# Kernel tuning notes

Hardware: AMD Instinct MI355X
Metric: run time of the kernel (lower is better)

## Reference

```python
import jax, jax.numpy as jnp
import numpy as np

N, E = 100000, 640000
IN_DIM, OUT_DIM, H, D = 128, 128, 4, 32  # head_dim = out_dim // num_heads
NUM_EDGE_TYPES = 3
NEG_SLOPE = 0.2


def setup_inputs() -> dict:
    key = jax.random.key(0)
    ks = jax.random.split(key, 10)
    x = jax.random.normal(ks[0], (N, IN_DIM), dtype=jnp.float32)
    edge_index = jax.random.randint(ks[1], (2, E), 0, N, dtype=jnp.int32)
    edge_type = jax.random.randint(ks[2], (E,), 0, NUM_EDGE_TYPES, dtype=jnp.int32)
    s = 1.0 / np.sqrt(IN_DIM)
    Wq = jax.random.uniform(ks[3], (IN_DIM, H * D), jnp.float32, -s, s)
    Wk = jax.random.uniform(ks[4], (IN_DIM, H * D), jnp.float32, -s, s)
    Wv = jax.random.uniform(ks[5], (IN_DIM, H * D), jnp.float32, -s, s)
    # xavier_uniform on (1, H, 2D): gain*sqrt(6/(fan_in+fan_out)) with fans (2D, H)
    a = np.sqrt(6.0 / (2 * D + H))
    attn_lin = jax.random.uniform(ks[6], (1, H, 2 * D), jnp.float32, -a, a)
    edge_embed_table = jax.random.normal(ks[7], (NUM_EDGE_TYPES, H * D), dtype=jnp.float32)
    so = 1.0 / np.sqrt(H * D)
    Wout = jax.random.uniform(ks[8], (H * D, OUT_DIM), jnp.float32, -so, so)
    bout = jax.random.uniform(ks[9], (OUT_DIM,), jnp.float32, -so, so)
    return {"x": x, "Wq": Wq, "Wk": Wk, "Wv": Wv, "attn_lin": attn_lin,
            "edge_embed_table": edge_embed_table, "Wout": Wout, "bout": bout,
            "edge_index": edge_index, "edge_type": edge_type}


def reference(x, Wq, Wk, Wv, attn_lin, edge_embed_table, Wout, bout, edge_index, edge_type):
    n = x.shape[0]
    src, dst = edge_index[0], edge_index[1]
    q = (x @ Wq).reshape(n, H, D)
    k = (x @ Wk).reshape(n, H, D)
    v = (x @ Wv).reshape(n, H, D)
    q_src = q[src]            # (E, H, D)
    k_dst = k[dst]            # (E, H, D)
    # (cat([q_src,k_dst]) * attn_lin).sum(-1) == q_src.a_q + k_dst.a_k
    a_q, a_k = attn_lin[0, :, :D], attn_lin[0, :, D:]      # (H, D) each
    scores = jnp.einsum('ehd,hd->eh', q_src, a_q) + jnp.einsum('ehd,hd->eh', k_dst, a_k)
    scores = jnp.where(scores >= 0, scores, NEG_SLOPE * scores)  # leaky_relu
    edge_embed = edge_embed_table[edge_type].reshape(-1, H, D)
    scores = scores + jnp.sum(q_src * edge_embed, axis=-1)       # (E, H)
    # segmented softmax over destination node (detached max, clamped at -100)
    m = jax.ops.segment_max(jax.lax.stop_gradient(scores), dst, num_segments=n)
    m = jnp.maximum(m, -100.0)
    ex = jnp.exp(scores - m[dst])
    denom = jax.ops.segment_sum(ex, dst, num_segments=n)
    alpha = ex / (denom[dst] + 1e-10)                            # (E, H)
    messages = alpha[:, :, None] * v[src]                        # (E, H, D)
    out = jax.ops.segment_sum(messages, dst, num_segments=n)     # (N, H, D)
    out = out.reshape(n, H * D)
    return out @ Wout + bout
```

## Files before the change

kernel.cpp:

```cpp
#include <hip/hip_runtime.h>
#include <hip/hip_bf16.h>

#define H_   4
#define D_   32
#define HD   128
#define IND  128
#define OUTD 128
#define NET  3
#define NEG  0.2f
#define CAP  2048

typedef short short8 __attribute__((ext_vector_type(8)));
typedef float f32x4  __attribute__((ext_vector_type(4)));

__device__ __forceinline__ unsigned short f2bf(float f) {
  union { __hip_bfloat16 b; unsigned short u; } x;
  x.b = __float2bfloat16(f);
  return x.u;
}

__device__ __forceinline__ short8 pack_bf8(float4 lo, float4 hi) {
  union { short8 s; unsigned short u[8]; } r;
  r.u[0] = f2bf(lo.x); r.u[1] = f2bf(lo.y); r.u[2] = f2bf(lo.z); r.u[3] = f2bf(lo.w);
  r.u[4] = f2bf(hi.x); r.u[5] = f2bf(hi.y); r.u[6] = f2bf(hi.z); r.u[7] = f2bf(hi.w);
  return r.s;
}

__global__ void k0b_pack(const float* __restrict__ Wq, const float* __restrict__ Wk,
                         const float* __restrict__ attn, const float* __restrict__ ee,
                         const float* __restrict__ Wv, const float* __restrict__ Wout,
                         unsigned short* __restrict__ Wallt,
                         unsigned short* __restrict__ Woutt,
                         int* __restrict__ gbuck, int nbuck) {
  int b = blockIdx.x, i = threadIdx.x;
  if (b == 288) {
    for (int k = i; k < nbuck; k += 128) gbuck[k] = 0;
    return;
  }
  if (b < 160) {
    int c = b;
    float val = 0.f;
    if (c < 128) {
      val = Wv[i*HD + c];
    } else {
      int cc = c - 128;
      if (cc < 4) {
        int h = cc;
        for (int d = 0; d < D_; d++) val += Wq[i*HD + h*D_ + d] * attn[h*2*D_ + d];
      } else if (cc < 16) {
        int t2 = (cc - 4) >> 2, h = (cc - 4) & 3;
        for (int d = 0; d < D_; d++) val += Wq[i*HD + h*D_ + d] * ee[t2*HD + h*D_ + d];
      } else if (cc < 20) {
        int h = cc - 16;
        for (int d = 0; d < D_; d++) val += Wk[i*HD + h*D_ + d] * attn[h*2*D_ + D_ + d];
      }
    }
    Wallt[(c*128 + i) ^ ((c & 7) << 3)] = f2bf(val);
  } else {
    int c = b - 160;
    Woutt[(c*128 + i) ^ ((c & 7) << 3)] = f2bf(Wout[i*OUTD + c]);
  }
}

__global__ __launch_bounds__(256) void k1_gemm(const float* __restrict__ x,
    const uint4* __restrict__ Wallt,
    unsigned short* __restrict__ vb, float* __restrict__ nq,
    float* __restrict__ skb, int n) {
  __shared__ uint4 ldsB[2560];
  int t = threadIdx.x;
  #pragma unroll
  for (int i = 0; i < 10; i++) ldsB[i*256 + t] = Wallt[i*256 + t];
  int wv = t >> 6, lane = t & 63;
  int l15 = lane & 15, l16 = lane >> 4;
  int base = blockIdx.x * 64;
  int arow = base + wv*16 + l15;
  int rr = min(arow, n - 1);
  const float* xr = &x[(size_t)rr*IND + l16*8];
  short8 afr[4];
  #pragma unroll
  for (int kk = 0; kk < 4; kk++) {
    float4 lo = *(const float4*)(xr + kk*32);
    float4 hi = *(const float4*)(xr + kk*32 + 4);
    afr[kk] = pack_bf8(lo, hi);
  }
  __syncthreads();
  f32x4 acc[10];
  #pragma unroll
  for (int nt = 0; nt < 10; nt++) acc[nt] = (f32x4){0.f, 0.f, 0.f, 0.f};
  #pragma unroll
  for (int nt = 0; nt < 10; nt++) {
    int bcol = nt*16 + l15;
    #pragma unroll
    for (int kk = 0; kk < 4; kk++) {
      int bytec = kk*64 + l16*16;
      short8 b = *(const short8*)((const char*)ldsB + ((bcol*256 + bytec) ^ ((bcol & 7) << 4)));
      acc[nt] = __builtin_amdgcn_mfma_f32_16x16x32_bf16(afr[kk], b, acc[nt], 0, 0, 0);
    }
  }
  int rowbase = base + wv*16 + l16*4;
  #pragma unroll
  for (int nt = 0; nt < 10; nt++) {
    int col = nt*16 + l15;
    #pragma unroll
    for (int r = 0; r < 4; r++) {
      int row = rowbase + r;
      if (row >= n) continue;
      float val = acc[nt][r];
      if (nt < 8)       vb[(size_t)row*HD + col] = f2bf(val);
      else if (nt == 8) nq[(size_t)row*16 + (col - 128)] = val;
      else { int c = col - 144; if (c < 4) skb[(size_t)row*4 + c] = val; }
    }
  }
}

__global__ __launch_bounds__(256) void k_bucket(const int* __restrict__ ei,
    const int* __restrict__ et, int* __restrict__ gbuck,
    unsigned int* __restrict__ ebuf, int E_, int nbuck, int per) {
  __shared__ int cnt[1024];
  __shared__ int base[1024];
  int t = threadIdx.x;
  for (int i = t; i < nbuck; i += 256) cnt[i] = 0;
  __syncthreads();
  int e0 = blockIdx.x * per;
  int e1 = min(e0 + per, E_);
  for (int e = e0 + t; e < e1; e += 256)
    atomicAdd(&cnt[ei[E_ + e] >> 7], 1);
  __syncthreads();
  for (int i = t; i < nbuck; i += 256) {
    int c = cnt[i];
    base[i] = c ? atomicAdd(&gbuck[i], c) : 0;
    cnt[i] = 0;
  }
  __syncthreads();
  for (int e = e0 + t; e < e1; e += 256) {
    int d = ei[E_ + e];
    int b = d >> 7;
    int pos = base[b] + atomicAdd(&cnt[b], 1);
    ebuf[(size_t)b * CAP + pos] =
        (unsigned)ei[e] | ((unsigned)et[e] << 17) | ((unsigned)(d & 127) << 19);
  }
}

__global__ __launch_bounds__(256) void k_sort(const unsigned int* __restrict__ ebuf,
    const int* __restrict__ gbuck, int* __restrict__ offsets,
    int* __restrict__ elist, int n, int E_) {
  __shared__ int cnt[128], cur[128], sc[128], red[256];
  int b = blockIdx.x, t = threadIdx.x;
  int part = 0;
  for (int i = t; i < b; i += 256) part += gbuck[i];
  red[t] = part; __syncthreads();
  for (int off = 128; off > 0; off >>= 1) {
    if (t < off) red[t] += red[t + off];
    __syncthreads();
  }
  int bb = red[0];
  int m = gbuck[b];
  if (b == 0 && t == 0) offsets[n] = E_;
  if (t < 128) cnt[t] = 0;
  __syncthreads();
  const unsigned int* eb = ebuf + (size_t)b * CAP;
  for (int i = t; i < m; i += 256)
    atomicAdd(&cnt[(eb[i] >> 19) & 127], 1);
  __syncthreads();
  if (t < 128) sc[t] = cnt[t];
  __syncthreads();
  for (int off = 1; off < 128; off <<= 1) {
    int v = (t >= off && t < 128) ? sc[t - off] : 0;
    __syncthreads();
    if (t < 128) sc[t] += v;
    __syncthreads();
  }
  if (t < 128) {
    int excl = sc[t] - cnt[t];
    cur[t] = excl;
    int dst = b * 128 + t;
    if (dst < n) offsets[dst] = bb + excl;
  }
  __syncthreads();
  for (int i = t; i < m; i += 256) {
    unsigned int w = eb[i];
    int dl = (w >> 19) & 127;
    int p = bb + atomicAdd(&cur[dl], 1);
    elist[p] = (int)((w & 0x1FFFFu) | (((w >> 17) & 3u) << 20));
  }
}

__global__ __launch_bounds__(256) void k3_agg(
    const int* __restrict__ offsets, const int* __restrict__ elist,
    const float* __restrict__ nq, const float* __restrict__ skb,
    const unsigned short* __restrict__ vb, unsigned short* __restrict__ aggb, int n) {
  int t = threadIdx.x;
  int g = t >> 4, s = t & 15;
  int dst = blockIdx.x * 16 + g;
  __shared__ float s_esc[16][17][4];
  __shared__ int s_src[16][17];
  if (dst >= n) return;
  int off0 = offsets[dst];
  int deg = offsets[dst + 1] - off0;
  int h = s >> 2;
  unsigned short* orow = &aggb[(size_t)dst*HD + s*8];
  if (deg == 0) {
    *(uint4*)orow = make_uint4(0u, 0u, 0u, 0u);
    return;
  }
  float4 sk4 = *(const float4*)(&skb[(size_t)dst*4]);
  float dp0 = 0.f, dp1 = 0.f, dp2 = 0.f, dp3 = 0.f;
  float a0=0.f,a1=0.f,a2=0.f,a3=0.f,a4=0.f,a5=0.f,a6=0.f,a7=0.f;
  for (int bas = 0; bas < deg; bas += 16) {
    int cnt = min(16, deg - bas);
    float e0 = 0.f, e1 = 0.f, e2 = 0.f, e3 = 0.f;
    int src = 0;
    if (s < cnt) {
      int p = elist[off0 + bas + s];
      src = p & 0xFFFFF;
      int ety = p >> 20;
      float4 sq4 = *(const float4*)(&nq[(size_t)src*16]);
      float4 qe4 = *(const float4*)(&nq[(size_t)src*16 + 4 + ety*4]);
      float s0 = sq4.x + sk4.x; s0 = (s0 >= 0.f ? s0 : NEG*s0) + qe4.x; e0 = __expf(s0);
      float s1 = sq4.y + sk4.y; s1 = (s1 >= 0.f ? s1 : NEG*s1) + qe4.y; e1 = __expf(s1);
      float s2 = sq4.z + sk4.z; s2 = (s2 >= 0.f ? s2 : NEG*s2) + qe4.z; e2 = __expf(s2);
      float s3 = sq4.w + sk4.w; s3 = (s3 >= 0.f ? s3 : NEG*s3) + qe4.w; e3 = __expf(s3);
      dp0 += e0; dp1 += e1; dp2 += e2; dp3 += e3;
    }
    s_src[g][s] = src;
    *(float4*)(&s_esc[g][s][0]) = make_float4(e0, e1, e2, e3);
    __builtin_amdgcn_wave_barrier();
    int e = 0;
    for (; e + 4 <= cnt; e += 4) {
      float al0 = s_esc[g][e+0][h], al1 = s_esc[g][e+1][h];
      float al2 = s_esc[g][e+2][h], al3 = s_esc[g][e+3][h];
      int se0 = s_src[g][e+0], se1 = s_src[g][e+1];
      int se2 = s_src[g][e+2], se3 = s_src[g][e+3];
      uint4 v0 = *(const uint4*)(vb + (size_t)se0*HD + s*8);
      uint4 v1 = *(const uint4*)(vb + (size_t)se1*HD + s*8);
      uint4 v2 = *(const uint4*)(vb + (size_t)se2*HD + s*8);
      uint4 v3 = *(const uint4*)(vb + (size_t)se3*HD + s*8);
      a0 += al0 * __uint_as_float(v0.x << 16);
      a1 += al0 * __uint_as_float(v0.x & 0xFFFF0000u);
      a2 += al0 * __uint_as_float(v0.y << 16);
      a3 += al0 * __uint_as_float(v0.y & 0xFFFF0000u);
      a4 += al0 * __uint_as_float(v0.z << 16);
      a5 += al0 * __uint_as_float(v0.z & 0xFFFF0000u);
      a6 += al0 * __uint_as_float(v0.w << 16);
      a7 += al0 * __uint_as_float(v0.w & 0xFFFF0000u);
      a0 += al1 * __uint_as_float(v1.x << 16);
      a1 += al1 * __uint_as_float(v1.x & 0xFFFF0000u);
      a2 += al1 * __uint_as_float(v1.y << 16);
      a3 += al1 * __uint_as_float(v1.y & 0xFFFF0000u);
      a4 += al1 * __uint_as_float(v1.z << 16);
      a5 += al1 * __uint_as_float(v1.z & 0xFFFF0000u);
      a6 += al1 * __uint_as_float(v1.w << 16);
      a7 += al1 * __uint_as_float(v1.w & 0xFFFF0000u);
      a0 += al2 * __uint_as_float(v2.x << 16);
      a1 += al2 * __uint_as_float(v2.x & 0xFFFF0000u);
      a2 += al2 * __uint_as_float(v2.y << 16);
      a3 += al2 * __uint_as_float(v2.y & 0xFFFF0000u);
      a4 += al2 * __uint_as_float(v2.z << 16);
      a5 += al2 * __uint_as_float(v2.z & 0xFFFF0000u);
      a6 += al2 * __uint_as_float(v2.w << 16);
      a7 += al2 * __uint_as_float(v2.w & 0xFFFF0000u);
      a0 += al3 * __uint_as_float(v3.x << 16);
      a1 += al3 * __uint_as_float(v3.x & 0xFFFF0000u);
      a2 += al3 * __uint_as_float(v3.y << 16);
      a3 += al3 * __uint_as_float(v3.y & 0xFFFF0000u);
      a4 += al3 * __uint_as_float(v3.z << 16);
      a5 += al3 * __uint_as_float(v3.z & 0xFFFF0000u);
      a6 += al3 * __uint_as_float(v3.w << 16);
      a7 += al3 * __uint_as_float(v3.w & 0xFFFF0000u);
    }
    for (; e < cnt; e++) {
      float a = s_esc[g][e][h];
      int se = s_src[g][e];
      uint4 vv = *(const uint4*)(vb + (size_t)se*HD + s*8);
      a0 += a * __uint_as_float(vv.x << 16);
      a1 += a * __uint_as_float(vv.x & 0xFFFF0000u);
      a2 += a * __uint_as_float(vv.y << 16);
      a3 += a * __uint_as_float(vv.y & 0xFFFF0000u);
      a4 += a * __uint_as_float(vv.z << 16);
      a5 += a * __uint_as_float(vv.z & 0xFFFF0000u);
      a6 += a * __uint_as_float(vv.w << 16);
      a7 += a * __uint_as_float(vv.w & 0xFFFF0000u);
    }
    __builtin_amdgcn_wave_barrier();
  }
  #pragma unroll
  for (int off = 1; off < 16; off <<= 1) {
    dp0 += __shfl_xor(dp0, off);
    dp1 += __shfl_xor(dp1, off);
    dp2 += __shfl_xor(dp2, off);
    dp3 += __shfl_xor(dp3, off);
  }
  float den = (h == 0) ? dp0 : (h == 1) ? dp1 : (h == 2) ? dp2 : dp3;
  float inv = 1.f / (den + 1e-10f);
  uint4 pk;
  pk.x = (unsigned)f2bf(a0*inv) | ((unsigned)f2bf(a1*inv) << 16);
  pk.y = (unsigned)f2bf(a2*inv) | ((unsigned)f2bf(a3*inv) << 16);
  pk.z = (unsigned)f2bf(a4*inv) | ((unsigned)f2bf(a5*inv) << 16);
  pk.w = (unsigned)f2bf(a6*inv) | ((unsigned)f2bf(a7*inv) << 16);
  *(uint4*)orow = pk;
}

__global__ __launch_bounds__(256) void k4_gemm(const unsigned short* __restrict__ aggb,
    const uint4* __restrict__ Woutt, const float* __restrict__ bout,
    float* __restrict__ out, int n) {
  __shared__ uint4 ldsB[2048];
  int t = threadIdx.x;
  #pragma unroll
  for (int i = 0; i < 8; i++) ldsB[i*256 + t] = Woutt[i*256 + t];
  int wv = t >> 6, lane = t & 63;
  int l15 = lane & 15, l16 = lane >> 4;
  int base = blockIdx.x * 64;
  int arow = base + wv*16 + l15;
  int rr = min(arow, n - 1);
  const unsigned short* ar = &aggb[(size_t)rr*HD + l16*8];
  short8 afr[4];
  #pragma unroll
  for (int kk = 0; kk < 4; kk++)
    afr[kk] = *(const short8*)(ar + kk*32);
  __syncthreads();
  f32x4 acc[8];
  #pragma unroll
  for (int nt = 0; nt < 8; nt++) acc[nt] = (f32x4){0.f, 0.f, 0.f, 0.f};
  #pragma unroll
  for (int nt = 0; nt < 8; nt++) {
    int bcol = nt*16 + l15;
    #pragma unroll
    for (int kk = 0; kk < 4; kk++) {
      int bytec = kk*64 + l16*16;
      short8 b = *(const short8*)((const char*)ldsB + ((bcol*256 + bytec) ^ ((bcol & 7) << 4)));
      acc[nt] = __builtin_amdgcn_mfma_f32_16x16x32_bf16(afr[kk], b, acc[nt], 0, 0, 0);
    }
  }
  int rowbase = base + wv*16 + l16*4;
  #pragma unroll
  for (int nt = 0; nt < 8; nt++) {
    int col = nt*16 + l15;
    float bv = bout[col];
    #pragma unroll
    for (int r = 0; r < 4; r++) {
      int row = rowbase + r;
      if (row < n) out[(size_t)row*OUTD + col] = acc[nt][r] + bv;
    }
  }
}

extern "C" void kernel_launch(void* const* d_in, const int* in_sizes, int n_in,
                              void* d_out, int out_size, void* d_ws, size_t ws_size,
                              hipStream_t stream) {
  const float* x    = (const float*)d_in[0];
  const float* Wq   = (const float*)d_in[1];
  const float* Wk   = (const float*)d_in[2];
  const float* Wv   = (const float*)d_in[3];
  const float* attn = (const float*)d_in[4];
  const float* ee   = (const float*)d_in[5];
  const float* Wout = (const float*)d_in[6];
  const float* bout = (const float*)d_in[7];
  const int*   ei   = (const int*)d_in[8];
  const int*   et   = (const int*)d_in[9];
  int n  = in_sizes[0] / IND;
  int E_ = in_sizes[9];
  float* out = (float*)d_out;
  int nbuck = (n + 127) >> 7;

  char* w = (char*)d_ws;
  auto alloc = [&](size_t bytes) {
    char* p = w;
    w += (bytes + 255) & ~(size_t)255;
    return p;
  };
  unsigned short* vb    = (unsigned short*)alloc((size_t)n * HD * 2);
  unsigned short* aggb  = (unsigned short*)alloc((size_t)n * HD * 2);
  float* nq       = (float*)alloc((size_t)n * 16 * 4);
  float* skb      = (float*)alloc((size_t)n * 4 * 4);
  unsigned short* Wallt = (unsigned short*)alloc(160 * 128 * 2);
  unsigned short* Woutt = (unsigned short*)alloc(128 * 128 * 2);
  unsigned int* ebuf = (unsigned int*)alloc((size_t)nbuck * CAP * 4);
  int*   gbuck    = (int*)alloc((size_t)nbuck * 4);
  int*   offsets  = (int*)alloc(((size_t)n + 1) * 4);
  int*   elist    = (int*)alloc((size_t)E_ * 4);

  k0b_pack<<<289, 128, 0, stream>>>(Wq, Wk, attn, ee, Wv, Wout, Wallt, Woutt,
                                    gbuck, nbuck);
  k1_gemm<<<(n + 63)/64, 256, 0, stream>>>(x, (const uint4*)Wallt, vb, nq, skb, n);
  int nbb = 256;
  int per = (E_ + nbb - 1) / nbb;
  k_bucket<<<nbb, 256, 0, stream>>>(ei, et, gbuck, ebuf, E_, nbuck, per);
  k_sort<<<nbuck, 256, 0, stream>>>(ebuf, gbuck, offsets, elist, n, E_);
  k3_agg<<<(n + 15)/16, 256, 0, stream>>>(offsets, elist, nq, skb, vb, aggb, n);
  k4_gemm<<<(n + 63)/64, 256, 0, stream>>>(aggb, (const uint4*)Woutt, bout, out, n);
}
```

Baseline: 107.0 us.

## Merge edge bucketing into projection GEMM launch and store node scores as bf16

The edge-bucketing kernel now runs as extra blocks of the projection GEMM launch, so the two independent stages share one launch and can overlap on the GPU. The per-node attention-score table nq is stored in bf16 instead of fp32, which halves the bytes gathered per edge in the aggregation kernel. Source offsets are also pre-shifted into row offsets so the inner gather loop does less address arithmetic. The bf16 scores lose precision before the exponent, and the dynamic 40 KB shared allocation applies to bucketing blocks too, which may limit occupancy.

```diff
diff --git a/kernel.cpp b/kernel.cpp
--- a/kernel.cpp
+++ b/kernel.cpp
@@ -25,6 +25,9 @@
   r.u[4] = f2bf(hi.x); r.u[5] = f2bf(hi.y); r.u[6] = f2bf(hi.z); r.u[7] = f2bf(hi.w);
   return r.s;
 }
+
+#define BFLO(x) __uint_as_float((x) << 16)
+#define BFHI(x) __uint_as_float((x) & 0xFFFF0000u)
 
 __global__ void k0b_pack(const float* __restrict__ Wq, const float* __restrict__ Wk,
                          const float* __restrict__ attn, const float* __restrict__ ee,
@@ -62,12 +65,42 @@
   }
 }
 
-__global__ __launch_bounds__(256) void k1_gemm(const float* __restrict__ x,
+__global__ __launch_bounds__(256) void k1b(const float* __restrict__ x,
     const uint4* __restrict__ Wallt,
-    unsigned short* __restrict__ vb, float* __restrict__ nq,
-    float* __restrict__ skb, int n) {
-  __shared__ uint4 ldsB[2560];
+    unsigned short* __restrict__ vb, unsigned short* __restrict__ nqb,
+    float* __restrict__ skb, int n, int nblk1,
+    const int* __restrict__ ei, const int* __restrict__ et,
+    int* __restrict__ gbuck, unsigned int* __restrict__ ebuf,
+    int E_, int nbuck, int per) {
+  extern __shared__ char dlds[];
   int t = threadIdx.x;
+  if (blockIdx.x >= nblk1) {
+    int* cnt  = (int*)dlds;
+    int* base = cnt + 1024;
+    for (int i = t; i < nbuck; i += 256) cnt[i] = 0;
+    __syncthreads();
+    int bb = blockIdx.x - nblk1;
+    int e0 = bb * per;
+    int e1 = min(e0 + per, E_);
+    for (int e = e0 + t; e < e1; e += 256)
+      atomicAdd(&cnt[ei[E_ + e] >> 7], 1);
+    __syncthreads();
+    for (int i = t; i < nbuck; i += 256) {
+      int c = cnt[i];
+      base[i] = c ? atomicAdd(&gbuck[i], c) : 0;
+      cnt[i] = 0;
+    }
+    __syncthreads();
+    for (int e = e0 + t; e < e1; e += 256) {
+      int d = ei[E_ + e];
+      int b = d >> 7;
+      int pos = base[b] + atomicAdd(&cnt[b], 1);
+      ebuf[(size_t)b * CAP + pos] =
+          (unsigned)ei[e] | ((unsigned)et[e] << 17) | ((unsigned)(d & 127) << 19);
+    }
+    return;
+  }
+  uint4* ldsB = (uint4*)dlds;
   #pragma unroll
   for (int i = 0; i < 10; i++) ldsB[i*256 + t] = Wallt[i*256 + t];
   int wv = t >> 6, lane = t & 63;
@@ -107,37 +140,9 @@
       if (row >= n) continue;
       float val = acc[nt][r];
       if (nt < 8)       vb[(size_t)row*HD + col] = f2bf(val);
-      else if (nt == 8) nq[(size_t)row*16 + (col - 128)] = val;
+      else if (nt == 8) nqb[((size_t)row << 4) + (col - 128)] = f2bf(val);
       else { int c = col - 144; if (c < 4) skb[(size_t)row*4 + c] = val; }
     }
-  }
-}
-
-__global__ __launch_bounds__(256) void k_bucket(const int* __restrict__ ei,
-    const int* __restrict__ et, int* __restrict__ gbuck,
-    unsigned int* __restrict__ ebuf, int E_, int nbuck, int per) {
-  __shared__ int cnt[1024];
-  __shared__ int base[1024];
-  int t = threadIdx.x;
-  for (int i = t; i < nbuck; i += 256) cnt[i] = 0;
-  __syncthreads();
-  int e0 = blockIdx.x * per;
-  int e1 = min(e0 + per, E_);
-  for (int e = e0 + t; e < e1; e += 256)
-    atomicAdd(&cnt[ei[E_ + e] >> 7], 1);
-  __syncthreads();
-  for (int i = t; i < nbuck; i += 256) {
-    int c = cnt[i];
-    base[i] = c ? atomicAdd(&gbuck[i], c) : 0;
-    cnt[i] = 0;
-  }
-  __syncthreads();
-  for (int e = e0 + t; e < e1; e += 256) {
-    int d = ei[E_ + e];
-    int b = d >> 7;
-    int pos = base[b] + atomicAdd(&cnt[b], 1);
-    ebuf[(size_t)b * CAP + pos] =
-        (unsigned)ei[e] | ((unsigned)et[e] << 17) | ((unsigned)(d & 127) << 19);
   }
 }
 
@@ -187,7 +192,7 @@
 
 __global__ __launch_bounds__(256) void k3_agg(
     const int* __restrict__ offsets, const int* __restrict__ elist,
-    const float* __restrict__ nq, const float* __restrict__ skb,
+    const unsigned short* __restrict__ nqb, const float* __restrict__ skb,
     const unsigned short* __restrict__ vb, unsigned short* __restrict__ aggb, int n) {
   int t = threadIdx.x;
   int g = t >> 4, s = t & 15;
@@ -209,77 +214,65 @@
   for (int bas = 0; bas < deg; bas += 16) {
     int cnt = min(16, deg - bas);
     float e0 = 0.f, e1 = 0.f, e2 = 0.f, e3 = 0.f;
-    int src = 0;
+    int srcoff = 0;
     if (s < cnt) {
       int p = elist[off0 + bas + s];
-      src = p & 0xFFFFF;
+      int src = p & 0xFFFFF;
       int ety = p >> 20;
-      float4 sq4 = *(const float4*)(&nq[(size_t)src*16]);
-      float4 qe4 = *(const float4*)(&nq[(size_t)src*16 + 4 + ety*4]);
-      float s0 = sq4.x + sk4.x; s0 = (s0 >= 0.f ? s0 : NEG*s0) + qe4.x; e0 = __expf(s0);
-      float s1 = sq4.y + sk4.y; s1 = (s1 >= 0.f ? s1 : NEG*s1) + qe4.y; e1 = __expf(s1);
-      float s2 = sq4.z + sk4.z; s2 = (s2 >= 0.f ? s2 : NEG*s2) + qe4.z; e2 = __expf(s2);
-      float s3 = sq4.w + sk4.w; s3 = (s3 >= 0.f ? s3 : NEG*s3) + qe4.w; e3 = __expf(s3);
+      const unsigned short* nr = nqb + ((size_t)src << 4);
+      uint2 sqp = *(const uint2*)nr;
+      uint2 qep = *(const uint2*)(nr + 4 + ety*4);
+      float s0 = BFLO(sqp.x) + sk4.x;
+      float s1 = BFHI(sqp.x) + sk4.y;
+      float s2 = BFLO(sqp.y) + sk4.z;
+      float s3 = BFHI(sqp.y) + sk4.w;
+      s0 = (s0 >= 0.f ? s0 : NEG*s0) + BFLO(qep.x); e0 = __expf(s0);
+      s1 = (s1 >= 0.f ? s1 : NEG*s1) + BFHI(qep.x); e1 = __expf(s1);
+      s2 = (s2 >= 0.f ? s2 : NEG*s2) + BFLO(qep.y); e2 = __expf(s2);
+      s3 = (s3 >= 0.f ? s3 : NEG*s3) + BFHI(qep.y); e3 = __expf(s3);
       dp0 += e0; dp1 += e1; dp2 += e2; dp3 += e3;
-    }
-    s_src[g][s] = src;
+      srcoff = src << 7;
+    }
+    s_src[g][s] = srcoff;
     *(float4*)(&s_esc[g][s][0]) = make_float4(e0, e1, e2, e3);
     __builtin_amdgcn_wave_barrier();
     int e = 0;
     for (; e + 4 <= cnt; e += 4) {
       float al0 = s_esc[g][e+0][h], al1 = s_esc[g][e+1][h];
       float al2 = s_esc[g][e+2][h], al3 = s_esc[g][e+3][h];
-      int se0 = s_src[g][e+0], se1 = s_src[g][e+1];
-      int se2 = s_src[g][e+2], se3 = s_src[g][e+3];
-      uint4 v0 = *(const uint4*)(vb + (size_t)se0*HD + s*8);
-      uint4 v1 = *(const uint4*)(vb + (size_t)se1*HD + s*8);
-      uint4 v2 = *(const uint4*)(vb + (size_t)se2*HD + s*8);
-      uint4 v3 = *(const uint4*)(vb + (size_t)se3*HD + s*8);
-      a0 += al0 * __uint_as_float(v0.x << 16);
-      a1 += al0 * __uint_as_float(v0.x & 0xFFFF0000u);
-      a2 += al0 * __uint_as_float(v0.y << 16);
-      a3 += al0 * __uint_as_float(v0.y & 0xFFFF0000u);
-      a4 += al0 * __uint_as_float(v0.z << 16);
-      a5 += al0 * __uint_as_float(v0.z & 0xFFFF0000u);
-      a6 += al0 * __uint_as_float(v0.w << 16);
-      a7 += al0 * __uint_as_float(v0.w & 0xFFFF0000u);
-      a0 += al1 * __uint_as_float(v1.x << 16);
-      a1 += al1 * __uint_as_float(v1.x & 0xFFFF0000u);
-      a2 += al1 * __uint_as_float(v1.y << 16);
-      a3 += al1 * __uint_as_float(v1.y & 0xFFFF0000u);
-      a4 += al1 * __uint_as_float(v1.z << 16);
-      a5 += al1 * __uint_as_float(v1.z & 0xFFFF0000u);
-      a6 += al1 * __uint_as_float(v1.w << 16);
-      a7 += al1 * __uint_as_float(v1.w & 0xFFFF0000u);
-      a0 += al2 * __uint_as_float(v2.x << 16);
-      a1 += al2 * __uint_as_float(v2.x & 0xFFFF0000u);
-      a2 += al2 * __uint_as_float(v2.y << 16);
-      a3 += al2 * __uint_as_float(v2.y & 0xFFFF0000u);
-      a4 += al2 * __uint_as_float(v2.z << 16);
-      a5 += al2 * __uint_as_float(v2.z & 0xFFFF0000u);
-      a6 += al2 * __uint_as_float(v2.w << 16);
-      a7 += al2 * __uint_as_float(v2.w & 0xFFFF0000u);
-      a0 += al3 * __uint_as_float(v3.x << 16);
-      a1 += al3 * __uint_as_float(v3.x & 0xFFFF0000u);
-      a2 += al3 * __uint_as_float(v3.y << 16);
-      a3 += al3 * __uint_as_float(v3.y & 0xFFFF0000u);
-      a4 += al3 * __uint_as_float(v3.z << 16);
-      a5 += al3 * __uint_as_float(v3.z & 0xFFFF0000u);
-      a6 += al3 * __uint_as_float(v3.w << 16);
-      a7 += al3 * __uint_as_float(v3.w & 0xFFFF0000u);
+      const unsigned short* p0 = vb + s_src[g][e+0] + s*8;
+      const unsigned short* p1 = vb + s_src[g][e+1] + s*8;
+      const unsigned short* p2 = vb + s_src[g][e+2] + s*8;
+      const unsigned short* p3 = vb + s_src[g][e+3] + s*8;
+      uint4 v0 = *(const uint4*)p0;
+      uint4 v1 = *(const uint4*)p1;
+      uint4 v2 = *(const uint4*)p2;
+      uint4 v3 = *(const uint4*)p3;
+      a0 += al0 * BFLO(v0.x); a1 += al0 * BFHI(v0.x);
+      a2 += al0 * BFLO(v0.y); a3 += al0 * BFHI(v0.y);
+      a4 += al0 * BFLO(v0.z); a5 += al0 * BFHI(v0.z);
+      a6 += al0 * BFLO(v0.w); a7 += al0 * BFHI(v0.w);
+      a0 += al1 * BFLO(v1.x); a1 += al1 * BFHI(v1.x);
+      a2 += al1 * BFLO(v1.y); a3 += al1 * BFHI(v1.y);
+      a4 += al1 * BFLO(v1.z); a5 += al1 * BFHI(v1.z);
+      a6 += al1 * BFLO(v1.w); a7 += al1 * BFHI(v1.w);
+      a0 += al2 * BFLO(v2.x); a1 += al2 * BFHI(v2.x);
+      a2 += al2 * BFLO(v2.y); a3 += al2 * BFHI(v2.y);
+      a4 += al2 * BFLO(v2.z); a5 += al2 * BFHI(v2.z);
+      a6 += al2 * BFLO(v2.w); a7 += al2 * BFHI(v2.w);
+      a0 += al3 * BFLO(v3.x); a1 += al3 * BFHI(v3.x);
+      a2 += al3 * BFLO(v3.y); a3 += al3 * BFHI(v3.y);
+      a4 += al3 * BFLO(v3.z); a5 += al3 * BFHI(v3.z);
+      a6 += al3 * BFLO(v3.w); a7 += al3 * BFHI(v3.w);
     }
     for (; e < cnt; e++) {
       float a = s_esc[g][e][h];
-      int se = s_src[g][e];
-      uint4 vv = *(const uint4*)(vb + (size_t)se*HD + s*8);
-      a0 += a * __uint_as_float(vv.x << 16);
-      a1 += a * __uint_as_float(vv.x & 0xFFFF0000u);
-      a2 += a * __uint_as_float(vv.y << 16);
-      a3 += a * __uint_as_float(vv.y & 0xFFFF0000u);
-      a4 += a * __uint_as_float(vv.z << 16);
-      a5 += a * __uint_as_float(vv.z & 0xFFFF0000u);
-      a6 += a * __uint_as_float(vv.w << 16);
-      a7 += a * __uint_as_float(vv.w & 0xFFFF0000u);
+      const unsigned short* p = vb + s_src[g][e] + s*8;
+      uint4 vv = *(const uint4*)p;
+      a0 += a * BFLO(vv.x); a1 += a * BFHI(vv.x);
+      a2 += a * BFLO(vv.y); a3 += a * BFHI(vv.y);
+      a4 += a * BFLO(vv.z); a5 += a * BFHI(vv.z);
+      a6 += a * BFLO(vv.w); a7 += a * BFHI(vv.w);
     }
     __builtin_amdgcn_wave_barrier();
   }
@@ -370,7 +363,7 @@
   };
   unsigned short* vb    = (unsigned short*)alloc((size_t)n * HD * 2);
   unsigned short* aggb  = (unsigned short*)alloc((size_t)n * HD * 2);
-  float* nq       = (float*)alloc((size_t)n * 16 * 4);
+  unsigned short* nqb   = (unsigned short*)alloc((size_t)n * 16 * 2);
   float* skb      = (float*)alloc((size_t)n * 4 * 4);
   unsigned short* Wallt = (unsigned short*)alloc(160 * 128 * 2);
   unsigned short* Woutt = (unsigned short*)alloc(128 * 128 * 2);
@@ -381,11 +374,13 @@
 
   k0b_pack<<<289, 128, 0, stream>>>(Wq, Wk, attn, ee, Wv, Wout, Wallt, Woutt,
                                     gbuck, nbuck);
-  k1_gemm<<<(n + 63)/64, 256, 0, stream>>>(x, (const uint4*)Wallt, vb, nq, skb, n);
+  int nblk1 = (n + 63) / 64;
   int nbb = 256;
   int per = (E_ + nbb - 1) / nbb;
-  k_bucket<<<nbb, 256, 0, stream>>>(ei, et, gbuck, ebuf, E_, nbuck, per);
+  k1b<<<nblk1 + nbb, 256, 40960, stream>>>(x, (const uint4*)Wallt, vb, nqb, skb,
+                                           n, nblk1, ei, et, gbuck, ebuf,
+                                           E_, nbuck, per);
   k_sort<<<nbuck, 256, 0, stream>>>(ebuf, gbuck, offsets, elist, n, E_);
-  k3_agg<<<(n + 15)/16, 256, 0, stream>>>(offsets, elist, nq, skb, vb, aggb, n);
+  k3_agg<<<(n + 15)/16, 256, 0, stream>>>(offsets, elist, nqb, skb, vb, aggb, n);
   k4_gemm<<<(n + 63)/64, 256, 0, stream>>>(aggb, (const uint4*)Woutt, bout, out, n);
 }
```

Measured after the change: 99.86 us. 1.07x faster.
